# Performance work log

Hardware: AMD Instinct MI355X
Metric: run time of the kernel (lower is better)

The kernel has to match this reference:

```python
import jax, jax.numpy as jnp
import numpy as np

N_PROBLEMS = 20000
N_SKILLS = 1000
EMB_SIZE = 128
TIME_LOG = 5.0
B, L = 64, 1024


def setup_inputs() -> dict:
    key = jax.random.key(0)
    ks = jax.random.split(key, 10)
    skills = jax.random.randint(ks[0], (B, L), 0, N_SKILLS)
    problems = jax.random.randint(ks[1], (B, L), 0, N_PROBLEMS)
    labels = jax.random.randint(ks[2], (B, L), 0, 2)
    times = jnp.sort(jax.random.randint(ks[3], (B, L), 0, 1_000_000), axis=-1)
    inp = jnp.stack([skills, problems, labels, times], axis=1)  # [B,4,L]
    std = 0.01
    return {
        "input": inp,
        "problem_base": std * jax.random.normal(ks[4], (N_PROBLEMS, 1), jnp.float32),
        "skill_base": std * jax.random.normal(ks[5], (N_SKILLS, 1), jnp.float32),
        "alpha_inter": std * jax.random.normal(ks[6], (N_SKILLS * 2, EMB_SIZE), jnp.float32),
        "alpha_skill": std * jax.random.normal(ks[7], (N_SKILLS, EMB_SIZE), jnp.float32),
        "beta_inter": std * jax.random.normal(ks[8], (N_SKILLS * 2, EMB_SIZE), jnp.float32),
        "beta_skill": std * jax.random.normal(ks[9], (N_SKILLS, EMB_SIZE), jnp.float32),
    }


def reference(input, problem_base, skill_base, alpha_inter, alpha_skill, beta_inter, beta_skill):
    skills = input[:, 0]    # [B,L]
    problems = input[:, 1]
    labels = input[:, 2]
    times = input[:, 3]

    mask_labels = labels * (labels < 2).astype(labels.dtype)
    inters = skills + mask_labels * N_SKILLS  # [B,L] in [0, 2*N_SKILLS)

    # pairwise Hawkes excitation / decay scores: [B,L,L]
    alphas = jnp.einsum('bie,bje->bij', alpha_inter[inters], alpha_skill[skills])
    betas = jnp.einsum('bie,bje->bij', beta_inter[inters], beta_skill[skills])
    betas = jnp.clip(betas + 1.0, 0.0, 10.0)

    dt = jnp.abs(times[:, :, None] - times[:, None, :]).astype(jnp.float32)
    log_dt = jnp.log(dt + 1e-10) / np.log(TIME_LOG)

    cross_effects = alphas * jnp.exp(-betas * log_dt)

    seq_len = skills.shape[1]
    # keep strictly-upper-triangular entries (source i before target j)
    keep = jnp.triu(jnp.ones((seq_len, seq_len), dtype=bool), k=1)
    sum_t = jnp.where(keep[None], cross_effects, 0.0).sum(axis=-2)  # [B,L]

    problem_bias = problem_base[problems][..., 0]
    skill_bias = skill_base[skills][..., 0]
    return jax.nn.sigmoid(problem_bias + skill_bias + sum_t)
```

## Files before the change

kernel.cpp:

```cpp
#include <hip/hip_runtime.h>
#include <hip/hip_bf16.h>

#define NB   64
#define SL   1024
#define EMB  128
#define NSK  1000
#define TI   64

#define TB_ELEMS 768000

#define AI_B 0
#define BI_B 512000
#define AS_B 1024000
#define BS_B 1280000

using short8  = __attribute__((ext_vector_type(8))) short;
using floatx4 = __attribute__((ext_vector_type(4))) float;

#define INV_LOG2_5 0.43067655807339306f

__device__ inline unsigned cvt2(float x, float y) {
    float2 f; f.x = x; f.y = y;
    __hip_bfloat162 h = __float22bfloat162_rn(f);
    unsigned u; __builtin_memcpy(&u, &h, sizeof(u));
    return u;
}

extern "C" __global__ __launch_bounds__(256)
void cvt_tables(const float* __restrict__ ai, const float* __restrict__ bi,
                const float* __restrict__ as, const float* __restrict__ bs,
                unsigned short* __restrict__ dst)
{
    const int t = blockIdx.x * 256 + threadIdx.x;
    const long e = (long)t * 8;
    const float* src;
    if      (e < 256000) src = ai + e;
    else if (e < 512000) src = bi + (e - 256000);
    else if (e < 640000) src = as + (e - 512000);
    else                 src = bs + (e - 640000);
    float4 f0 = *(const float4*)src;
    float4 f1 = *(const float4*)(src + 4);
    uint4 pk;
    pk.x = cvt2(f0.x, f0.y); pk.y = cvt2(f0.z, f0.w);
    pk.z = cvt2(f1.x, f1.y); pk.w = cvt2(f1.z, f1.w);
    *(uint4*)(dst + e) = pk;
}

__device__ float fixup_pair(const float* __restrict__ air,
                            const float* __restrict__ bir,
                            const float* __restrict__ asr,
                            const float* __restrict__ bsr) {
    float da = 0.f, db = 0.f;
#pragma unroll 8
    for (int k = 0; k < EMB; k += 4) {
        float4 a  = *(const float4*)(air + k);
        float4 s  = *(const float4*)(asr + k);
        float4 bq = *(const float4*)(bir + k);
        float4 tt = *(const float4*)(bsr + k);
        da += a.x * s.x + a.y * s.y + a.z * s.z + a.w * s.w;
        db += bq.x * tt.x + bq.y * tt.y + bq.z * tt.z + bq.w * tt.w;
    }
    float beta = fminf(fmaxf(db + 1.f, 0.f), 10.f);
    return da * __expf(beta * 14.30676558073393f);
}

struct StageH { uint4 q0, q1, q2, q3; };

__device__ __forceinline__ StageH stageh_load(const int* __restrict__ binp,
                                              const char* __restrict__ tbc,
                                              int half, int row, long matb, int sq)
{
    const int arow = half * 32 + row;
    const long intr = binp[arow] + (long)binp[2 * SL + arow] * NSK;
    const char* p = tbc + matb + intr * 256 + sq * 64;
    StageH s;
    s.q0 = *(const uint4*)(p);      s.q1 = *(const uint4*)(p + 16);
    s.q2 = *(const uint4*)(p + 32); s.q3 = *(const uint4*)(p + 48);
    return s;
}

__device__ __forceinline__ void stageh_write(char* buf, int row, long matoff,
                                             int wslot, const StageH& s)
{
    char* p  = buf + matoff + row * 256 + wslot;
    char* px = buf + matoff + row * 256 + (wslot ^ 16);
    *(uint4*)(p)        = s.q0;  *(uint4*)(p + 128)  = s.q1;
    *(uint4*)(px)       = s.q2;  *(uint4*)(px + 128) = s.q3;
}

extern "C" __global__ __launch_bounds__(256, 4)
void hawkes_fused(const int*   __restrict__ inp,
                  const unsigned short* __restrict__ tb,
                  const float* __restrict__ pbase,
                  const float* __restrict__ sbase,
                  const float* __restrict__ ai, const float* __restrict__ as,
                  const float* __restrict__ bi, const float* __restrict__ bs,
                  float*       __restrict__ out)
{
    __shared__ uint4 ldsq[2048];
    char* ldsc = (char*)ldsq;

    const int bid  = blockIdx.x;
    const int b    = bid & (NB - 1);
    const int jt   = 15 - (bid >> 6);
    const int tid  = threadIdx.x;
    const int w    = tid >> 6;
    const int l    = tid & 63;
    const int quad = l >> 4;
    const int col  = l & 15;

    const int* __restrict__ binp = inp + b * 4 * SL;
    const char* __restrict__ tbc = (const char*)tb;

    const int jlane = jt * TI + w * 16 + col;
    const int sk_j  = binp[jlane];
    const int tj    = binp[3 * SL + jlane];

    short8 bfa[4], bfb[4];
    {
        const char* asr = tbc + AS_B + (long)sk_j * 256 + quad * 16;
        const char* bsr = tbc + BS_B + (long)sk_j * 256 + quad * 16;
#pragma unroll
        for (int ks = 0; ks < 4; ++ks) {
            bfa[ks] = *(const short8*)(asr + ks * 64);
            bfb[ks] = *(const short8*)(bsr + ks * 64);
        }
    }

    const int  srow  = tid >> 3;
    const long matb  = ((tid >> 2) & 1) ? (long)BI_B : (long)AI_B;
    const long matoff = ((tid >> 2) & 1) ? 8192 : 0;
    const int  sq    = tid & 3;
    const int  wslot = (((2 * sq) ^ (srow & 7)) << 4);

    int roff[4];
    {
        const int qh = quad >> 1, ql = quad & 1, c7 = col & 7;
#pragma unroll
        for (int ks = 0; ks < 4; ++ks)
            roff[ks] = col * 256 + ql * 128 + (((2 * ks + qh) ^ c7) << 4);
    }

    const int nh = 2 * (jt + 1);
    float sum = 0.f;

    StageH sEven = stageh_load(binp, tbc, 0, srow, matb, sq);
    stageh_write(ldsc, srow, matoff, wslot, sEven);
    StageH sOdd;
    if (nh > 1) sOdd = stageh_load(binp, tbc, 1, srow, matb, sq);

#pragma unroll 1
    for (int t = 0; t <= jt; ++t) {
        const int h2 = 2 * t + 2;

#pragma unroll
        for (int ph = 0; ph < 2; ++ph) {
            __syncthreads();
            if (ph == 0) {
                stageh_write(ldsc + 16384, srow, matoff, wslot, sOdd);
                if (h2 < nh) sEven = stageh_load(binp, tbc, h2, srow, matb, sq);
            } else {
                if (h2 < nh)     stageh_write(ldsc, srow, matoff, wslot, sEven);
                if (h2 + 1 < nh) sOdd = stageh_load(binp, tbc, h2 + 1, srow, matb, sq);
            }

            const char* buf     = ldsc + (ph ? 16384 : 0);
            const int   rowbase = t * 64 + ph * 32;

#pragma unroll
            for (int isub = 0; isub < 2; ++isub) {
                short8 av[4], bv[4];
#pragma unroll
                for (int ks = 0; ks < 4; ++ks) {
                    av[ks] = *(const short8*)(buf + isub * 4096 + roff[ks]);
                    bv[ks] = *(const short8*)(buf + 8192 + isub * 4096 + roff[ks]);
                }
                const int4 t4 = *(const int4*)(binp + 3 * SL + rowbase + isub * 16 + quad * 4);

                floatx4 aa = {0.f, 0.f, 0.f, 0.f};
                floatx4 bb = {1.f, 1.f, 1.f, 1.f};
#pragma unroll
                for (int ks = 0; ks < 4; ++ks) {
                    aa = __builtin_amdgcn_mfma_f32_16x16x32_bf16(av[ks], bfa[ks], aa, 0, 0, 0);
                    bb = __builtin_amdgcn_mfma_f32_16x16x32_bf16(bv[ks], bfb[ks], bb, 0, 0, 0);
                }
#pragma unroll
                for (int rr = 0; rr < 4; ++rr) {
                    const int ti = (rr == 0) ? t4.x : (rr == 1) ? t4.y : (rr == 2) ? t4.z : t4.w;
                    const int dt = tj - ti;
                    float lc  = __log2f((float)dt);
                    float nb  = fminf(fmaxf(bb[rr], 0.f), 10.f) * (-INV_LOG2_5);
                    float arg = (dt > 0) ? nb * lc : -__builtin_inff();
                    sum += aa[rr] * __builtin_amdgcn_exp2f(arg);
                }
            }
        }
    }

    sum += __shfl_xor(sum, 16, 64);
    sum += __shfl_xor(sum, 32, 64);

    if (quad == 0) {
        float corr = 0.f;
        for (int i = jlane - 1; i >= 0 && binp[3 * SL + i] == tj; --i) {
            const int ski = binp[i], li = binp[2 * SL + i];
            const long intr = ski + (long)li * NSK;
            corr += fixup_pair(ai + intr * EMB, bi + intr * EMB,
                               as + (long)sk_j * EMB, bs + (long)sk_j * EMB);
        }
        const float x = pbase[binp[SL + jlane]] + sbase[sk_j] + sum + corr;
        out[b * SL + jlane] = 1.f / (1.f + __expf(-x));
    }
}

extern "C" void kernel_launch(void* const* d_in, const int* in_sizes, int n_in,
                              void* d_out, int out_size, void* d_ws, size_t ws_size,
                              hipStream_t stream) {
    const int*   inp = (const int*)d_in[0];
    const float* pb  = (const float*)d_in[1];
    const float* sb  = (const float*)d_in[2];
    const float* ai  = (const float*)d_in[3];
    const float* as  = (const float*)d_in[4];
    const float* bi  = (const float*)d_in[5];
    const float* bs  = (const float*)d_in[6];

    unsigned short* tb = (unsigned short*)d_ws;

    cvt_tables<<<dim3(96000 / 256), dim3(256), 0, stream>>>(ai, bi, as, bs, tb);
    hawkes_fused<<<dim3(16 * NB), dim3(256), 0, stream>>>(
        inp, tb, pb, sb, ai, as, bi, bs, (float*)d_out);
}
```

Baseline: 115.0 us.

## Fuse bf16 table conversion into main kernel and reorder tile scheduling

Drops the separate fp32-to-bf16 table conversion kernel. The main kernel now loads fp32 rows directly and converts them to bf16 in registers before writing to LDS. This removes one launch and a full pass over the tables, but doubles the global bytes fetched per staged row and raises register pressure (8 float4 per stage, double-buffered). It also replaces the descending jt block order with a fixed interleaved pattern, to balance the triangular work across CUs.

After: 321.5 us. 180% more time.

```diff
diff --git a/kernel.cpp b/kernel.cpp
--- a/kernel.cpp
+++ b/kernel.cpp
@@ -7,43 +7,18 @@
 #define NSK  1000
 #define TI   64
 
-#define TB_ELEMS 768000
-
-#define AI_B 0
-#define BI_B 512000
-#define AS_B 1024000
-#define BS_B 1280000
-
 using short8  = __attribute__((ext_vector_type(8))) short;
 using floatx4 = __attribute__((ext_vector_type(4))) float;
 
 #define INV_LOG2_5 0.43067655807339306f
+
+#define JT_PATTERN 0x75318ACE64209BDFULL
 
 __device__ inline unsigned cvt2(float x, float y) {
     float2 f; f.x = x; f.y = y;
     __hip_bfloat162 h = __float22bfloat162_rn(f);
     unsigned u; __builtin_memcpy(&u, &h, sizeof(u));
     return u;
-}
-
-extern "C" __global__ __launch_bounds__(256)
-void cvt_tables(const float* __restrict__ ai, const float* __restrict__ bi,
-                const float* __restrict__ as, const float* __restrict__ bs,
-                unsigned short* __restrict__ dst)
-{
-    const int t = blockIdx.x * 256 + threadIdx.x;
-    const long e = (long)t * 8;
-    const float* src;
-    if      (e < 256000) src = ai + e;
-    else if (e < 512000) src = bi + (e - 256000);
-    else if (e < 640000) src = as + (e - 512000);
-    else                 src = bs + (e - 640000);
-    float4 f0 = *(const float4*)src;
-    float4 f1 = *(const float4*)(src + 4);
-    uint4 pk;
-    pk.x = cvt2(f0.x, f0.y); pk.y = cvt2(f0.z, f0.w);
-    pk.z = cvt2(f1.x, f1.y); pk.w = cvt2(f1.z, f1.w);
-    *(uint4*)(dst + e) = pk;
 }
 
 __device__ float fixup_pair(const float* __restrict__ air,
@@ -64,33 +39,42 @@
     return da * __expf(beta * 14.30676558073393f);
 }
 
-struct StageH { uint4 q0, q1, q2, q3; };
-
-__device__ __forceinline__ StageH stageh_load(const int* __restrict__ binp,
-                                              const char* __restrict__ tbc,
-                                              int half, int row, long matb, int sq)
+struct StageF { float4 f0, f1, f2, f3, f4, f5, f6, f7; };
+
+__device__ __forceinline__ StageF stagef_load(const int* __restrict__ binp,
+                                              const float* __restrict__ mat,
+                                              int half, int row, int sq)
 {
     const int arow = half * 32 + row;
     const long intr = binp[arow] + (long)binp[2 * SL + arow] * NSK;
-    const char* p = tbc + matb + intr * 256 + sq * 64;
-    StageH s;
-    s.q0 = *(const uint4*)(p);      s.q1 = *(const uint4*)(p + 16);
-    s.q2 = *(const uint4*)(p + 32); s.q3 = *(const uint4*)(p + 48);
+    const float* p = mat + intr * (long)EMB + sq * 32;
+    StageF s;
+    s.f0 = *(const float4*)(p);      s.f1 = *(const float4*)(p + 4);
+    s.f2 = *(const float4*)(p + 8);  s.f3 = *(const float4*)(p + 12);
+    s.f4 = *(const float4*)(p + 16); s.f5 = *(const float4*)(p + 20);
+    s.f6 = *(const float4*)(p + 24); s.f7 = *(const float4*)(p + 28);
     return s;
 }
 
-__device__ __forceinline__ void stageh_write(char* buf, int row, long matoff,
-                                             int wslot, const StageH& s)
+__device__ __forceinline__ void stageh_write_cvt(char* buf, int row, long matoff,
+                                                 int wslot, const StageF& f)
 {
+    const uint4 q0 = make_uint4(cvt2(f.f0.x, f.f0.y), cvt2(f.f0.z, f.f0.w),
+                                cvt2(f.f1.x, f.f1.y), cvt2(f.f1.z, f.f1.w));
+    const uint4 q1 = make_uint4(cvt2(f.f2.x, f.f2.y), cvt2(f.f2.z, f.f2.w),
+                                cvt2(f.f3.x, f.f3.y), cvt2(f.f3.z, f.f3.w));
+    const uint4 q2 = make_uint4(cvt2(f.f4.x, f.f4.y), cvt2(f.f4.z, f.f4.w),
+                                cvt2(f.f5.x, f.f5.y), cvt2(f.f5.z, f.f5.w));
+    const uint4 q3 = make_uint4(cvt2(f.f6.x, f.f6.y), cvt2(f.f6.z, f.f6.w),
+                                cvt2(f.f7.x, f.f7.y), cvt2(f.f7.z, f.f7.w));
     char* p  = buf + matoff + row * 256 + wslot;
     char* px = buf + matoff + row * 256 + (wslot ^ 16);
-    *(uint4*)(p)        = s.q0;  *(uint4*)(p + 128)  = s.q1;
-    *(uint4*)(px)       = s.q2;  *(uint4*)(px + 128) = s.q3;
+    *(uint4*)(p)        = q0;  *(uint4*)(p + 128)  = q1;
+    *(uint4*)(px)       = q2;  *(uint4*)(px + 128) = q3;
 }
 
 extern "C" __global__ __launch_bounds__(256, 4)
 void hawkes_fused(const int*   __restrict__ inp,
-                  const unsigned short* __restrict__ tb,
                   const float* __restrict__ pbase,
                   const float* __restrict__ sbase,
                   const float* __restrict__ ai, const float* __restrict__ as,
@@ -102,7 +86,7 @@
 
     const int bid  = blockIdx.x;
     const int b    = bid & (NB - 1);
-    const int jt   = 15 - (bid >> 6);
+    const int jt   = (int)((JT_PATTERN >> ((bid >> 6) << 2)) & 15);
     const int tid  = threadIdx.x;
     const int w    = tid >> 6;
     const int l    = tid & 63;
@@ -110,7 +94,6 @@
     const int col  = l & 15;
 
     const int* __restrict__ binp = inp + b * 4 * SL;
-    const char* __restrict__ tbc = (const char*)tb;
 
     const int jlane = jt * TI + w * 16 + col;
     const int sk_j  = binp[jlane];
@@ -118,20 +101,31 @@
 
     short8 bfa[4], bfb[4];
     {
-        const char* asr = tbc + AS_B + (long)sk_j * 256 + quad * 16;
-        const char* bsr = tbc + BS_B + (long)sk_j * 256 + quad * 16;
+        const float* asr = as + (long)sk_j * EMB + quad * 8;
+        const float* bsr = bs + (long)sk_j * EMB + quad * 8;
+        union UF { uint4 u; short8 s8; };
 #pragma unroll
         for (int ks = 0; ks < 4; ++ks) {
-            bfa[ks] = *(const short8*)(asr + ks * 64);
-            bfb[ks] = *(const short8*)(bsr + ks * 64);
+            float4 a0 = *(const float4*)(asr + ks * 32);
+            float4 a1 = *(const float4*)(asr + ks * 32 + 4);
+            float4 b0 = *(const float4*)(bsr + ks * 32);
+            float4 b1 = *(const float4*)(bsr + ks * 32 + 4);
+            UF ua, ub;
+            ua.u = make_uint4(cvt2(a0.x, a0.y), cvt2(a0.z, a0.w),
+                              cvt2(a1.x, a1.y), cvt2(a1.z, a1.w));
+            ub.u = make_uint4(cvt2(b0.x, b0.y), cvt2(b0.z, b0.w),
+                              cvt2(b1.x, b1.y), cvt2(b1.z, b1.w));
+            bfa[ks] = ua.s8;
+            bfb[ks] = ub.s8;
         }
     }
 
-    const int  srow  = tid >> 3;
-    const long matb  = ((tid >> 2) & 1) ? (long)BI_B : (long)AI_B;
-    const long matoff = ((tid >> 2) & 1) ? 8192 : 0;
-    const int  sq    = tid & 3;
-    const int  wslot = (((2 * sq) ^ (srow & 7)) << 4);
+    const int   srow   = tid >> 3;
+    const int   mymat  = (tid >> 2) & 1;
+    const float* smat  = mymat ? bi : ai;
+    const long  matoff = mymat ? 8192 : 0;
+    const int   sq     = tid & 3;
+    const int   wslot  = (((2 * sq) ^ (srow & 7)) << 4);
 
     int roff[4];
     {
@@ -144,10 +138,10 @@
     const int nh = 2 * (jt + 1);
     float sum = 0.f;
 
-    StageH sEven = stageh_load(binp, tbc, 0, srow, matb, sq);
-    stageh_write(ldsc, srow, matoff, wslot, sEven);
-    StageH sOdd;
-    if (nh > 1) sOdd = stageh_load(binp, tbc, 1, srow, matb, sq);
+    StageF sEven = stagef_load(binp, smat, 0, srow, sq);
+    stageh_write_cvt(ldsc, srow, matoff, wslot, sEven);
+    StageF sOdd;
+    if (nh > 1) sOdd = stagef_load(binp, smat, 1, srow, sq);
 
 #pragma unroll 1
     for (int t = 0; t <= jt; ++t) {
@@ -157,11 +151,11 @@
         for (int ph = 0; ph < 2; ++ph) {
             __syncthreads();
             if (ph == 0) {
-                stageh_write(ldsc + 16384, srow, matoff, wslot, sOdd);
-                if (h2 < nh) sEven = stageh_load(binp, tbc, h2, srow, matb, sq);
+                stageh_write_cvt(ldsc + 16384, srow, matoff, wslot, sOdd);
+                if (h2 < nh) sEven = stagef_load(binp, smat, h2, srow, sq);
             } else {
-                if (h2 < nh)     stageh_write(ldsc, srow, matoff, wslot, sEven);
-                if (h2 + 1 < nh) sOdd = stageh_load(binp, tbc, h2 + 1, srow, matb, sq);
+                if (h2 < nh)     stageh_write_cvt(ldsc, srow, matoff, wslot, sEven);
+                if (h2 + 1 < nh) sOdd = stagef_load(binp, smat, h2 + 1, srow, sq);
             }
 
             const char* buf     = ldsc + (ph ? 16384 : 0);
@@ -224,9 +218,6 @@
     const float* bi  = (const float*)d_in[5];
     const float* bs  = (const float*)d_in[6];
 
-    unsigned short* tb = (unsigned short*)d_ws;
-
-    cvt_tables<<<dim3(96000 / 256), dim3(256), 0, stream>>>(ai, bi, as, bs, tb);
     hawkes_fused<<<dim3(16 * NB), dim3(256), 0, stream>>>(
-        inp, tb, pb, sb, ai, as, bi, bs, (float*)d_out);
-}
+        inp, pb, sb, ai, as, bi, bs, (float*)d_out);
+}
```
